# Optimization experiments

Hardware: AMD Instinct MI355X
Metric: run time of the kernel (lower is better)

Reference implementation:

```python
import jax, jax.numpy as jnp
import numpy as np

N_NODES = 50000
N_EDGES = 600000
IN_DIM = 128
FEAT = 128
N_CLS = 40


def _lin_params(key, fan_in, fan_out, bias=True):
    k1, k2 = jax.random.split(key)
    lim = 1.0 / np.sqrt(fan_in)
    W = jax.random.uniform(k1, (fan_out, fan_in), jnp.float32, -lim, lim)
    b = jax.random.uniform(k2, (fan_out,), jnp.float32, -lim, lim) if bias else None
    return W, b


def setup_inputs() -> dict:
    key = jax.random.key(0)
    ks = jax.random.split(key, 8)
    x = jax.random.normal(ks[0], (N_NODES, IN_DIM), jnp.float32)
    edge_index = jax.random.randint(ks[1], (2, N_EDGES), 0, N_NODES, jnp.int64 if jax.config.read('jax_enable_x64') else jnp.int32)
    Wl1, bl1 = _lin_params(ks[2], IN_DIM, FEAT)
    Wr1, _ = _lin_params(ks[3], IN_DIM, FEAT, bias=False)
    Wl2, bl2 = _lin_params(ks[4], FEAT, FEAT)
    Wr2, _ = _lin_params(ks[5], FEAT, FEAT, bias=False)
    Wl3, bl3 = _lin_params(ks[6], FEAT, FEAT)
    Wr3, _ = _lin_params(ks[7], FEAT, FEAT, bias=False)
    kc = jax.random.fold_in(key, 99)
    Wc, bc = _lin_params(kc, FEAT, N_CLS)
    return {"x": x, "edge_index": edge_index,
            "Wl1": Wl1, "bl1": bl1, "Wr1": Wr1,
            "Wl2": Wl2, "bl2": bl2, "Wr2": Wr2,
            "Wl3": Wl3, "bl3": bl3, "Wr3": Wr3,
            "Wc": Wc, "bc": bc}


def _sage_relu(x, src, dst, deg_inv, Wl, bl, Wr):
    # mean aggregation over incoming neighbors: gather at src, scatter-add at dst
    agg = jax.ops.segment_sum(x[src], dst, num_segments=N_NODES)  # [N, F]
    agg = agg * deg_inv[:, None]
    out = agg @ Wl.T + bl + x @ Wr.T  # W1*mean(neigh) + W2*x_root
    return jax.nn.relu(out)


def reference(x, edge_index, Wl1, bl1, Wr1, Wl2, bl2, Wr2, Wl3, bl3, Wr3, Wc, bc):
    src, dst = edge_index[0], edge_index[1]
    deg = jax.ops.segment_sum(jnp.ones((src.shape[0],), x.dtype), dst, num_segments=N_NODES)
    deg_inv = 1.0 / jnp.maximum(deg, 1.0)
    local_repr = _sage_relu(x, src, dst, deg_inv, Wl1, bl1, Wr1)
    global_repr = _sage_relu(local_repr, src, dst, deg_inv, Wl2, bl2, Wr2)
    # invariant_feature_extractor: one SAGEConvwithRelu + (eval-mode) dropout + residual
    h = _sage_relu(global_repr, src, dst, deg_inv, Wl3, bl3, Wr3)
    vanilla_if = h + global_repr
    vanilla_pred = vanilla_if @ Wc.T + bc
    return vanilla_pred
```

## Files before the change

kernel.cpp:

```cpp
#include <hip/hip_runtime.h>
#include <hip/hip_bf16.h>

constexpr int N_NODES = 50000;
constexpr int N_EDGES = 600000;
constexpr int D       = 128;
constexpr int N_CLS   = 40;

constexpr float QS = 2048.0f;
constexpr float DQ = 1.0f / 2048.0f;

using bf16x8 = __attribute__((ext_vector_type(8))) short;
using f32x4  = __attribute__((ext_vector_type(4))) float;

__device__ inline unsigned short f2bf(float f) {
    __hip_bfloat16 h = __float2bfloat16(f);
    return __builtin_bit_cast(unsigned short, h);
}
__device__ inline float bf2f(unsigned short u) {
    __hip_bfloat16 h = __builtin_bit_cast(__hip_bfloat16, u);
    return __bfloat162float(h);
}
__device__ inline short q16(float v) {
    float s = v * QS;
    s = fminf(fmaxf(s, -32767.f), 32767.f);
    return (short)__float2int_rn(s);
}


__global__ void hist_kernel(const int* __restrict__ ei, int* __restrict__ cnt) {
    int e = blockIdx.x * 256 + threadIdx.x;
    if (e < N_EDGES) atomicAdd(&cnt[ei[N_EDGES + e]], 1);
}

__global__ __launch_bounds__(1024) void scan_block_kernel(const int* __restrict__ cnt,
                                                          int* __restrict__ rs,
                                                          int* __restrict__ bsum, int n) {
    __shared__ int t[1024];
    int tid = threadIdx.x;
    int gid = blockIdx.x * 1024 + tid;
    int v = (gid < n) ? cnt[gid] : 0;
    t[tid] = v;
    __syncthreads();
    for (int off = 1; off < 1024; off <<= 1) {
        int u = (tid >= off) ? t[tid - off] : 0;
        __syncthreads();
        t[tid] += u;
        __syncthreads();
    }
    if (gid < n) rs[gid] = t[tid] - v;
    if (tid == 1023) bsum[blockIdx.x] = t[1023];
}

__global__ void finalize2_kernel(const int* __restrict__ cnt, int* __restrict__ rs,
                                 int* __restrict__ cursor, float* __restrict__ dinv,
                                 const int* __restrict__ bsum) {
    __shared__ int chunk_off;
    int tid = threadIdx.x;
    int i = blockIdx.x * 256 + tid;
    int chunk = blockIdx.x >> 2;
    if (tid < 64) {
        int v = (tid < chunk) ? bsum[tid] : 0;
#pragma unroll
        for (int o = 1; o < 64; o <<= 1) v += __shfl_xor(v, o);
        if (tid == 0) chunk_off = v;
    }
    __syncthreads();
    if (i < N_NODES) {
        int v = rs[i] + chunk_off;
        rs[i] = v;
        cursor[i] = v;
        dinv[i] = 1.0f / fmaxf((float)cnt[i], 1.0f);
        if (i == 0) rs[N_NODES] = N_EDGES;
    }
}

__global__ void scatter_kernel(const int* __restrict__ ei, int* __restrict__ cursor,
                               int* __restrict__ csr) {
    int e = blockIdx.x * 256 + threadIdx.x;
    if (e < N_EDGES) {
        int d = ei[N_EDGES + e];
        int p = atomicAdd(&cursor[d], 1);
        csr[p] = ei[e];
    }
}

__global__ void split_w3_kernel(const float* __restrict__ Wl1, const float* __restrict__ Wr1,
                                const float* __restrict__ Wl2, const float* __restrict__ Wr2,
                                const float* __restrict__ Wl3, const float* __restrict__ Wr3,
                                unsigned short* __restrict__ hi, unsigned short* __restrict__ lo) {
    int layer = blockIdx.x >> 7;
    int idx = (blockIdx.x & 127) * 256 + threadIdx.x;
    int n = idx >> 8, k = idx & 255;
    const float* Wl = (layer == 0) ? Wl1 : (layer == 1) ? Wl2 : Wl3;
    const float* Wr = (layer == 0) ? Wr1 : (layer == 1) ? Wr2 : Wr3;
    float v = (k < 128) ? Wl[n * 128 + k] : Wr[n * 128 + (k - 128)];
    unsigned short h = f2bf(v);
    size_t o = (size_t)layer * 32768 + idx;
    hi[o] = h;
    lo[o] = f2bf(v - bf2f(h));
}

__global__ void split_wc_kernel(const float* __restrict__ Wc,
                                unsigned short* __restrict__ hi, unsigned short* __restrict__ lo) {
    int idx = blockIdx.x * 256 + threadIdx.x;
    int n = idx >> 7, k = idx & 127;
    float v = (n < N_CLS) ? Wc[n * 128 + k] : 0.f;
    unsigned short h = f2bf(v);
    hi[idx] = h;
    lo[idx] = f2bf(v - bf2f(h));
}

__global__ __launch_bounds__(256) void agg_kernel(const float* __restrict__ feat,
                                                  const int* __restrict__ rs,
                                                  const int* __restrict__ csr,
                                                  const float* __restrict__ dinv,
                                                  float* __restrict__ aggn) {
    int wave = threadIdx.x >> 6;
    int lane = threadIdx.x & 63;
    int node = blockIdx.x * 4 + wave;
    if (node >= N_NODES) return;
    int e0 = rs[node], e1 = rs[node + 1];
    int half = lane >> 5;
    int fl = lane & 31;
    float ax = 0.f, ay = 0.f, az = 0.f, aw = 0.f;

    for (int base = e0; base < e1; base += 64) {
        int cnt = min(64, e1 - base);
        int idxv = (lane < cnt) ? csr[base + lane] : 0;
        int cnt2 = cnt & ~1;
        int j = 0;
        for (; j + 8 <= cnt2; j += 8) {
            int s0 = __shfl(idxv, j + half);
            int s1 = __shfl(idxv, j + 2 + half);
            int s2 = __shfl(idxv, j + 4 + half);
            int s3 = __shfl(idxv, j + 6 + half);
            float4 v0 = *(const float4*)&feat[(size_t)s0 * D + fl * 4];
            float4 v1 = *(const float4*)&feat[(size_t)s1 * D + fl * 4];
            float4 v2 = *(const float4*)&feat[(size_t)s2 * D + fl * 4];
            float4 v3 = *(const float4*)&feat[(size_t)s3 * D + fl * 4];
            ax += v0.x + v1.x + v2.x + v3.x;
            ay += v0.y + v1.y + v2.y + v3.y;
            az += v0.z + v1.z + v2.z + v3.z;
            aw += v0.w + v1.w + v2.w + v3.w;
        }
        for (; j < cnt2; j += 2) {
            int s = __shfl(idxv, j + half);
            float4 v = *(const float4*)&feat[(size_t)s * D + fl * 4];
            ax += v.x; ay += v.y; az += v.z; aw += v.w;
        }
        if (j < cnt) {
            int s = __shfl(idxv, j);
            if (half == 0) {
                float4 v = *(const float4*)&feat[(size_t)s * D + fl * 4];
                ax += v.x; ay += v.y; az += v.z; aw += v.w;
            }
        }
    }
    ax += __shfl(ax, lane ^ 32);
    ay += __shfl(ay, lane ^ 32);
    az += __shfl(az, lane ^ 32);
    aw += __shfl(aw, lane ^ 32);
    if (half == 0) {
        float di = dinv[node];
        float4 o; o.x = ax * di; o.y = ay * di; o.z = az * di; o.w = aw * di;
        *(float4*)&aggn[(size_t)node * D + fl * 4] = o;
    }
}

__global__ __launch_bounds__(256) void agg_q_kernel(const short* __restrict__ feat16,
                                                    const int* __restrict__ rs,
                                                    const int* __restrict__ csr,
                                                    const float* __restrict__ dinv,
                                                    float* __restrict__ aggn) {
    int wave = threadIdx.x >> 6;
    int lane = threadIdx.x & 63;
    int node = blockIdx.x * 4 + wave;
    if (node >= N_NODES) return;
    int e0 = rs[node], e1 = rs[node + 1];
    int q = lane >> 4;
    int fl = lane & 15;
    int acc[8] = {0, 0, 0, 0, 0, 0, 0, 0};

    auto acc8 = [&](uint4 u) {
        acc[0] += (int)(short)(u.x & 0xffff);
        acc[1] += (int)(short)(u.x >> 16);
        acc[2] += (int)(short)(u.y & 0xffff);
        acc[3] += (int)(short)(u.y >> 16);
        acc[4] += (int)(short)(u.z & 0xffff);
        acc[5] += (int)(short)(u.z >> 16);
        acc[6] += (int)(short)(u.w & 0xffff);
        acc[7] += (int)(short)(u.w >> 16);
    };

    for (int base = e0; base < e1; base += 64) {
        int cnt = min(64, e1 - base);
        int idxv = (lane < cnt) ? csr[base + lane] : 0;
        int bulk = cnt & ~15;
        int j = 0;
        for (; j < bulk; j += 16) {
            int s0 = __shfl(idxv, j + q);
            int s1 = __shfl(idxv, j + 4 + q);
            int s2 = __shfl(idxv, j + 8 + q);
            int s3 = __shfl(idxv, j + 12 + q);
            uint4 a = *(const uint4*)&feat16[(size_t)s0 * D + fl * 8];
            uint4 b = *(const uint4*)&feat16[(size_t)s1 * D + fl * 8];
            uint4 c = *(const uint4*)&feat16[(size_t)s2 * D + fl * 8];
            uint4 d = *(const uint4*)&feat16[(size_t)s3 * D + fl * 8];
            acc8(a); acc8(b); acc8(c); acc8(d);
        }
        for (; j < cnt; j += 4) {
            if (j + q < cnt) {
                int s = __shfl(idxv, j + q);
                uint4 a = *(const uint4*)&feat16[(size_t)s * D + fl * 8];
                acc8(a);
            }
        }
    }
#pragma unroll
    for (int i = 0; i < 8; ++i) {
        acc[i] += __shfl(acc[i], lane ^ 16);
        acc[i] += __shfl(acc[i], lane ^ 32);
    }
    if (q == 0) {
        float sc = dinv[node] * DQ;
        float4 o0, o1;
        o0.x = acc[0] * sc; o0.y = acc[1] * sc; o0.z = acc[2] * sc; o0.w = acc[3] * sc;
        o1.x = acc[4] * sc; o1.y = acc[5] * sc; o1.z = acc[6] * sc; o1.w = acc[7] * sc;
        *(float4*)&aggn[(size_t)node * D + fl * 8] = o0;
        *(float4*)&aggn[(size_t)node * D + fl * 8 + 4] = o1;
    }
}

__global__ __launch_bounds__(256) void gemm_mfma_kernel(const float* __restrict__ Aagg,
                                                        const float* __restrict__ Ax,
                                                        const unsigned short* __restrict__ Whi,
                                                        const unsigned short* __restrict__ Wlo,
                                                        const float* __restrict__ bias,
                                                        short* __restrict__ out16,
                                                        float* __restrict__ outp, int M) {
    __shared__ __align__(16) unsigned short AhS[64 * 32];
    __shared__ __align__(16) unsigned short AlS[64 * 32];
    __shared__ __align__(16) unsigned short WhS[128 * 32];
    __shared__ __align__(16) unsigned short WlS[128 * 32];
    char* AhB = (char*)AhS;
    char* AlB = (char*)AlS;
    char* WhB = (char*)WhS;
    char* WlB = (char*)WlS;

    int tid = threadIdx.x;
    int lane = tid & 63;
    int wid = tid >> 6;
    int wr = wid >> 1;
    int wc = wid & 1;
    int lr = lane & 15;
    int kg = (lane >> 4) * 8;
    int row0 = blockIdx.x * 64;

    f32x4 acc[2][4];
#pragma unroll
    for (int f = 0; f < 2; ++f)
#pragma unroll
        for (int j = 0; j < 4; ++j) acc[f][j] = (f32x4){0.f, 0.f, 0.f, 0.f};

    for (int kt = 0; kt < 8; ++kt) {
        const float* Asrc = (kt < 4) ? Aagg : Ax;
        int kcol = (kt & 3) * 32;

        {
            int row = tid >> 2;
            int k8 = (tid & 3) * 8;
            int gr = row0 + row;
            if (gr >= M) gr = M - 1;
            const float* p = &Asrc[(size_t)gr * D + kcol + k8];
            float4 v0 = *(const float4*)p;
            float4 v1 = *(const float4*)(p + 4);
            float fv[8] = {v0.x, v0.y, v0.z, v0.w, v1.x, v1.y, v1.z, v1.w};
            union { unsigned short u[8]; uint4 q; } ph, pl;
#pragma unroll
            for (int j = 0; j < 8; ++j) {
                unsigned short h = f2bf(fv[j]);
                ph.u[j] = h;
                pl.u[j] = f2bf(fv[j] - bf2f(h));
            }
            int boff = (row << 6) + (k8 << 1);
            boff ^= (row & 7) << 4;
            *(uint4*)(AhB + boff) = ph.q;
            *(uint4*)(AlB + boff) = pl.q;
        }
#pragma unroll
        for (int it = 0; it < 2; ++it) {
            int slot = tid + it * 256;
            int n = slot >> 2;
            int k8 = (slot & 3) * 8;
            size_t gsrc = (size_t)n * 256 + kt * 32 + k8;
            uint4 h = *(const uint4*)&Whi[gsrc];
            uint4 l = *(const uint4*)&Wlo[gsrc];
            int boff = (n << 6) + (k8 << 1);
            boff ^= (n & 7) << 4;
            *(uint4*)(WhB + boff) = h;
            *(uint4*)(WlB + boff) = l;
        }
        __syncthreads();

        {
            bf16x8 ah[2], al[2];
#pragma unroll
            for (int f = 0; f < 2; ++f) {
                int row = wr * 32 + f * 16 + lr;
                int boff = (row << 6) + (kg << 1);
                boff ^= (row & 7) << 4;
                ah[f] = *(const bf16x8*)(AhB + boff);
                al[f] = *(const bf16x8*)(AlB + boff);
            }
            bf16x8 bh[4], bl[4];
#pragma unroll
            for (int j = 0; j < 4; ++j) {
                int n = wc * 64 + j * 16 + lr;
                int boff = (n << 6) + (kg << 1);
                boff ^= (n & 7) << 4;
                bh[j] = *(const bf16x8*)(WhB + boff);
                bl[j] = *(const bf16x8*)(WlB + boff);
            }
#pragma unroll
            for (int f = 0; f < 2; ++f)
#pragma unroll
                for (int j = 0; j < 4; ++j) {
                    acc[f][j] = __builtin_amdgcn_mfma_f32_16x16x32_bf16(ah[f], bh[j], acc[f][j], 0, 0, 0);
                    acc[f][j] = __builtin_amdgcn_mfma_f32_16x16x32_bf16(ah[f], bl[j], acc[f][j], 0, 0, 0);
                    acc[f][j] = __builtin_amdgcn_mfma_f32_16x16x32_bf16(al[f], bh[j], acc[f][j], 0, 0, 0);
                }
        }
        __syncthreads();
    }

#pragma unroll
    for (int f = 0; f < 2; ++f)
#pragma unroll
        for (int j = 0; j < 4; ++j) {
            int c = wc * 64 + j * 16 + lr;
            float b = bias[c];
#pragma unroll
            for (int r = 0; r < 4; ++r) {
                int gr = row0 + wr * 32 + f * 16 + (lane >> 4) * 4 + r;
                if (gr < M) {
                    float v = fmaxf(acc[f][j][r] + b, 0.f);
                    outp[(size_t)gr * D + c] = v;
                    if (out16) out16[(size_t)gr * D + c] = q16(v);
                }
            }
        }
}

__global__ __launch_bounds__(256) void gemm_cls_kernel(const float* __restrict__ Aagg,
                                                       const float* __restrict__ Ax,
                                                       const unsigned short* __restrict__ Whi,
                                                       const unsigned short* __restrict__ Wlo,
                                                       const float* __restrict__ bias,
                                                       const float* __restrict__ residf,
                                                       const unsigned short* __restrict__ Wch,
                                                       const unsigned short* __restrict__ Wcl,
                                                       const float* __restrict__ bc,
                                                       float* __restrict__ outp, int M) {
    __shared__ __align__(16) char smem[49152];
    char* AhB = smem;
    char* AlB = smem + 8192;
    char* WhB = smem + 16384;
    char* WlB = smem + 32768;

    int tid = threadIdx.x;
    int lane = tid & 63;
    int wid = tid >> 6;
    int wr = wid >> 1;
    int wc = wid & 1;
    int lr = lane & 15;
    int kg = (lane >> 4) * 8;
    int row0 = blockIdx.x * 64;

    f32x4 acc[2][4];
#pragma unroll
    for (int f = 0; f < 2; ++f)
#pragma unroll
        for (int j = 0; j < 4; ++j) acc[f][j] = (f32x4){0.f, 0.f, 0.f, 0.f};

    for (int kt = 0; kt < 4; ++kt) {
        const float* Asrc = (kt < 2) ? Aagg : Ax;
        int kcol = (kt & 1) * 64;
#pragma unroll
        for (int it = 0; it < 2; ++it) {
            int slot = tid + it * 256;
            int row = slot >> 3;
            int k8 = (slot & 7) * 8;
            int gr = row0 + row;
            if (gr >= M) gr = M - 1;
            const float* p = &Asrc[(size_t)gr * D + kcol + k8];
            float4 v0 = *(const float4*)p;
            float4 v1 = *(const float4*)(p + 4);
            float fv[8] = {v0.x, v0.y, v0.z, v0.w, v1.x, v1.y, v1.z, v1.w};
            union { unsigned short u[8]; uint4 q; } ph, pl;
#pragma unroll
            for (int j = 0; j < 8; ++j) {
                unsigned short h = f2bf(fv[j]);
                ph.u[j] = h;
                pl.u[j] = f2bf(fv[j] - bf2f(h));
            }
            int boff = (row << 7) + (k8 << 1);
            boff ^= (row & 7) << 4;
            *(uint4*)(AhB + boff) = ph.q;
            *(uint4*)(AlB + boff) = pl.q;
        }
#pragma unroll
        for (int it = 0; it < 4; ++it) {
            int slot = tid + it * 256;
            int n = slot >> 3;
            int k8 = (slot & 7) * 8;
            size_t gsrc = (size_t)n * 256 + kt * 64 + k8;
            uint4 h = *(const uint4*)&Whi[gsrc];
            uint4 l = *(const uint4*)&Wlo[gsrc];
            int boff = (n << 7) + (k8 << 1);
            boff ^= (n & 7) << 4;
            *(uint4*)(WhB + boff) = h;
            *(uint4*)(WlB + boff) = l;
        }
        __syncthreads();
#pragma unroll
        for (int ks = 0; ks < 2; ++ks) {
            int kk = ks * 32 + kg;
            bf16x8 ah[2], al[2];
#pragma unroll
            for (int f = 0; f < 2; ++f) {
                int row = wr * 32 + f * 16 + lr;
                int boff = (row << 7) + (kk << 1);
                boff ^= (row & 7) << 4;
                ah[f] = *(const bf16x8*)(AhB + boff);
                al[f] = *(const bf16x8*)(AlB + boff);
            }
            bf16x8 bh[4], bl[4];
#pragma unroll
            for (int j = 0; j < 4; ++j) {
                int n = wc * 64 + j * 16 + lr;
                int boff = (n << 7) + (kk << 1);
                boff ^= (n & 7) << 4;
                bh[j] = *(const bf16x8*)(WhB + boff);
                bl[j] = *(const bf16x8*)(WlB + boff);
            }
#pragma unroll
            for (int f = 0; f < 2; ++f)
#pragma unroll
                for (int j = 0; j < 4; ++j) {
                    acc[f][j] = __builtin_amdgcn_mfma_f32_16x16x32_bf16(ah[f], bh[j], acc[f][j], 0, 0, 0);
                    acc[f][j] = __builtin_amdgcn_mfma_f32_16x16x32_bf16(ah[f], bl[j], acc[f][j], 0, 0, 0);
                    acc[f][j] = __builtin_amdgcn_mfma_f32_16x16x32_bf16(al[f], bh[j], acc[f][j], 0, 0, 0);
                }
        }
        __syncthreads();
    }

    f32x4 acc2[3];
#pragma unroll
    for (int j = 0; j < 3; ++j) acc2[j] = (f32x4){0.f, 0.f, 0.f, 0.f};

    for (int p = 0; p < 2; ++p) {
#pragma unroll
        for (int it = 0; it < 2; ++it) {
            int slot = tid + it * 256;
            if (slot < 384) {
                int n = slot >> 3;
                int k8 = (slot & 7) * 8;
                size_t gsrc = (size_t)n * 128 + p * 64 + k8;
                uint4 h = *(const uint4*)&Wch[gsrc];
                uint4 l = *(const uint4*)&Wcl[gsrc];
                int boff = (n << 7) + (k8 << 1);
                boff ^= (n & 7) << 4;
                *(uint4*)(WhB + boff) = h;
                *(uint4*)(WlB + boff) = l;
            }
        }
        if (wc == p) {
#pragma unroll
            for (int f = 0; f < 2; ++f)
#pragma unroll
                for (int j = 0; j < 4; ++j) {
                    int c = wc * 64 + j * 16 + lr;
                    float b = bias[c];
#pragma unroll
                    for (int r = 0; r < 4; ++r) {
                        int row = wr * 32 + f * 16 + (lane >> 4) * 4 + r;
                        int gr = row0 + row;
                        int gra = (gr < M) ? gr : (M - 1);
                        float v = fmaxf(acc[f][j][r] + b, 0.f);
                        v += residf[(size_t)gra * D + c];
                        int kloc = j * 16 + lr;
                        int boff = (row << 7) + (kloc << 1);
                        boff ^= (row & 7) << 4;
                        unsigned short h = f2bf(v);
                        *(unsigned short*)(AhB + boff) = h;
                        *(unsigned short*)(AlB + boff) = f2bf(v - bf2f(h));
                    }
                }
        }
        __syncthreads();

#pragma unroll
        for (int ks = 0; ks < 2; ++ks) {
            int kk = ks * 32 + kg;
            int row = wid * 16 + lr;
            int boffA = (row << 7) + (kk << 1);
            boffA ^= (row & 7) << 4;
            bf16x8 ah = *(const bf16x8*)(AhB + boffA);
            bf16x8 al = *(const bf16x8*)(AlB + boffA);
#pragma unroll
            for (int j = 0; j < 3; ++j) {
                int n = j * 16 + lr;
                int boffB = (n << 7) + (kk << 1);
                boffB ^= (n & 7) << 4;
                bf16x8 bh = *(const bf16x8*)(WhB + boffB);
                bf16x8 bl = *(const bf16x8*)(WlB + boffB);
                acc2[j] = __builtin_amdgcn_mfma_f32_16x16x32_bf16(ah, bh, acc2[j], 0, 0, 0);
                acc2[j] = __builtin_amdgcn_mfma_f32_16x16x32_bf16(ah, bl, acc2[j], 0, 0, 0);
                acc2[j] = __builtin_amdgcn_mfma_f32_16x16x32_bf16(al, bh, acc2[j], 0, 0, 0);
            }
        }
        __syncthreads();
    }

#pragma unroll
    for (int j = 0; j < 3; ++j) {
        int c = j * 16 + lr;
        if (c < N_CLS) {
            float b = bc[c];
#pragma unroll
            for (int r = 0; r < 4; ++r) {
                int gr = row0 + wid * 16 + (lane >> 4) * 4 + r;
                if (gr < M) outp[(size_t)gr * N_CLS + c] = acc2[j][r] + b;
            }
        }
    }
}

extern "C" void kernel_launch(void* const* d_in, const int* in_sizes, int n_in,
                              void* d_out, int out_size, void* d_ws, size_t ws_size,
                              hipStream_t stream) {
    const float* x   = (const float*)d_in[0];
    const int*   ei  = (const int*)d_in[1];
    const float* Wl1 = (const float*)d_in[2];
    const float* bl1 = (const float*)d_in[3];
    const float* Wr1 = (const float*)d_in[4];
    const float* Wl2 = (const float*)d_in[5];
    const float* bl2 = (const float*)d_in[6];
    const float* Wr2 = (const float*)d_in[7];
    const float* Wl3 = (const float*)d_in[8];
    const float* bl3 = (const float*)d_in[9];
    const float* Wr3 = (const float*)d_in[10];
    const float* Wc  = (const float*)d_in[11];
    const float* bc  = (const float*)d_in[12];
    float* out = (float*)d_out;

    char* w = (char*)d_ws;
    size_t off = 0;
    auto carve = [&](size_t bytes) -> void* {
        void* p = w + off;
        off = (off + bytes + 255) & ~(size_t)255;
        return p;
    };
    int*   cnt    = (int*)carve((size_t)N_NODES * 4);
    int*   rs     = (int*)carve((size_t)(N_NODES + 1) * 4);
    int*   cursor = (int*)carve((size_t)N_NODES * 4);
    float* dinv   = (float*)carve((size_t)N_NODES * 4);
    int*   bsum   = (int*)carve(64 * 4);
    int*   csr    = (int*)carve((size_t)N_EDGES * 4);
    float* aggn   = (float*)carve((size_t)N_NODES * D * 4);
    float* bufA   = (float*)carve((size_t)N_NODES * D * 4);
    float* bufB   = (float*)carve((size_t)N_NODES * D * 4);
    short* t16    = (short*)carve((size_t)N_NODES * D * 2);
    unsigned short* w123h = (unsigned short*)carve(3 * 128 * 256 * 2);
    unsigned short* w123l = (unsigned short*)carve(3 * 128 * 256 * 2);
    unsigned short* wch   = (unsigned short*)carve(48 * 128 * 2);
    unsigned short* wcl   = (unsigned short*)carve(48 * 128 * 2);
    (void)ws_size;

    const int NBLK_SCAN = (N_NODES + 1023) / 1024;
    const int GRID_E = (N_EDGES + 255) / 256;
    const int GRID_N = (N_NODES + 255) / 256;
    const int GRID_AGG = (N_NODES + 3) / 4;
    const int GRID_GEMM = (N_NODES + 63) / 64;

    hipMemsetAsync(cnt, 0, (size_t)N_NODES * 4, stream);
    hipLaunchKernelGGL(hist_kernel, dim3(GRID_E), dim3(256), 0, stream, ei, cnt);
    hipLaunchKernelGGL(split_w3_kernel, dim3(384), dim3(256), 0, stream,
                       Wl1, Wr1, Wl2, Wr2, Wl3, Wr3, w123h, w123l);
    hipLaunchKernelGGL(split_wc_kernel, dim3(24), dim3(256), 0, stream, Wc, wch, wcl);
    hipLaunchKernelGGL(scan_block_kernel, dim3(NBLK_SCAN), dim3(1024), 0, stream, cnt, rs, bsum, N_NODES);
    hipLaunchKernelGGL(finalize2_kernel, dim3(GRID_N), dim3(256), 0, stream, cnt, rs, cursor, dinv, bsum);
    hipLaunchKernelGGL(scatter_kernel, dim3(GRID_E), dim3(256), 0, stream, ei, cursor, csr);

    hipLaunchKernelGGL(agg_kernel, dim3(GRID_AGG), dim3(256), 0, stream, x, rs, csr, dinv, aggn);
    hipLaunchKernelGGL(gemm_mfma_kernel, dim3(GRID_GEMM), dim3(256), 0, stream,
                       aggn, x, w123h, w123l, bl1, (short*)nullptr, bufA, N_NODES);
    hipLaunchKernelGGL(agg_kernel, dim3(GRID_AGG), dim3(256), 0, stream, bufA, rs, csr, dinv, aggn);
    hipLaunchKernelGGL(gemm_mfma_kernel, dim3(GRID_GEMM), dim3(256), 0, stream,
                       aggn, bufA, w123h + 32768, w123l + 32768, bl2, t16, bufB, N_NODES);
    hipLaunchKernelGGL(agg_q_kernel, dim3(GRID_AGG), dim3(256), 0, stream, t16, rs, csr, dinv, aggn);
    hipLaunchKernelGGL(gemm_cls_kernel, dim3(GRID_GEMM), dim3(256), 0, stream,
                       aggn, bufB, w123h + 65536, w123l + 65536, bl3, bufB,
                       wch, wcl, bc, out, N_NODES);
}
```

Measured before the change: 341.4 us.

## Prefetch GEMM operands into registers and double-buffer A tile in LDS

The layer GEMM kernel stops staging weights through shared memory. Each wave now loads its bf16 hi/lo weight fragments straight from global memory into registers. A and weight loads for the next k-tile are issued before the MFMAs of the current tile, A is double-buffered in LDS, and the two barriers per iteration become one. The aim is to hide global load latency and cut LDS traffic and synchronisation, at the cost of more registers and redundant weight reads across waves, which rely on L1/L2.

```diff
diff --git a/kernel.cpp b/kernel.cpp
--- a/kernel.cpp
+++ b/kernel.cpp
@@ -231,21 +231,15 @@
     }
 }
 
-__global__ __launch_bounds__(256) void gemm_mfma_kernel(const float* __restrict__ Aagg,
-                                                        const float* __restrict__ Ax,
-                                                        const unsigned short* __restrict__ Whi,
-                                                        const unsigned short* __restrict__ Wlo,
-                                                        const float* __restrict__ bias,
-                                                        short* __restrict__ out16,
-                                                        float* __restrict__ outp, int M) {
-    __shared__ __align__(16) unsigned short AhS[64 * 32];
-    __shared__ __align__(16) unsigned short AlS[64 * 32];
-    __shared__ __align__(16) unsigned short WhS[128 * 32];
-    __shared__ __align__(16) unsigned short WlS[128 * 32];
-    char* AhB = (char*)AhS;
-    char* AlB = (char*)AlS;
-    char* WhB = (char*)WhS;
-    char* WlB = (char*)WlS;
+__global__ __launch_bounds__(256) void gemm_v2_kernel(const float* __restrict__ Aagg,
+                                                      const float* __restrict__ Ax,
+                                                      const unsigned short* __restrict__ Whi,
+                                                      const unsigned short* __restrict__ Wlo,
+                                                      const float* __restrict__ bias,
+                                                      short* __restrict__ out16,
+                                                      float* __restrict__ outp, int M) {
+    __shared__ __align__(16) unsigned short AhS[2][64 * 32];
+    __shared__ __align__(16) unsigned short AlS[2][64 * 32];
 
     int tid = threadIdx.x;
     int lane = tid & 63;
@@ -256,25 +250,46 @@
     int kg = (lane >> 4) * 8;
     int row0 = blockIdx.x * 64;
 
+    int arow = tid >> 2;
+    int ak8 = (tid & 3) * 8;
+    int agr = row0 + arow;
+    if (agr >= M) agr = M - 1;
+    const float* aag = &Aagg[(size_t)agr * D + ak8];
+    const float* axp = &Ax[(size_t)agr * D + ak8];
+    int aboff = (arow << 6) + (ak8 << 1);
+    aboff ^= (arow & 7) << 4;
+
+    const unsigned short* whp[4];
+    const unsigned short* wlp[4];
+#pragma unroll
+    for (int j = 0; j < 4; ++j) {
+        int n = wc * 64 + j * 16 + lr;
+        whp[j] = &Whi[n * 256 + kg];
+        wlp[j] = &Wlo[n * 256 + kg];
+    }
+
     f32x4 acc[2][4];
 #pragma unroll
     for (int f = 0; f < 2; ++f)
 #pragma unroll
         for (int j = 0; j < 4; ++j) acc[f][j] = (f32x4){0.f, 0.f, 0.f, 0.f};
 
+    float4 a0c = *(const float4*)(aag);
+    float4 a1c = *(const float4*)(aag + 4);
+    bf16x8 whc[4], wlc[4];
+#pragma unroll
+    for (int j = 0; j < 4; ++j) {
+        whc[j] = *(const bf16x8*)(whp[j]);
+        wlc[j] = *(const bf16x8*)(wlp[j]);
+    }
+
+#pragma unroll
     for (int kt = 0; kt < 8; ++kt) {
-        const float* Asrc = (kt < 4) ? Aagg : Ax;
-        int kcol = (kt & 3) * 32;
+        unsigned short* AhB = AhS[kt & 1];
+        unsigned short* AlB = AlS[kt & 1];
 
         {
-            int row = tid >> 2;
-            int k8 = (tid & 3) * 8;
-            int gr = row0 + row;
-            if (gr >= M) gr = M - 1;
-            const float* p = &Asrc[(size_t)gr * D + kcol + k8];
-            float4 v0 = *(const float4*)p;
-            float4 v1 = *(const float4*)(p + 4);
-            float fv[8] = {v0.x, v0.y, v0.z, v0.w, v1.x, v1.y, v1.z, v1.w};
+            float fv[8] = {a0c.x, a0c.y, a0c.z, a0c.w, a1c.x, a1c.y, a1c.z, a1c.w};
             union { unsigned short u[8]; uint4 q; } ph, pl;
 #pragma unroll
             for (int j = 0; j < 8; ++j) {
@@ -282,25 +297,29 @@
                 ph.u[j] = h;
                 pl.u[j] = f2bf(fv[j] - bf2f(h));
             }
-            int boff = (row << 6) + (k8 << 1);
-            boff ^= (row & 7) << 4;
-            *(uint4*)(AhB + boff) = ph.q;
-            *(uint4*)(AlB + boff) = pl.q;
-        }
-#pragma unroll
-        for (int it = 0; it < 2; ++it) {
-            int slot = tid + it * 256;
-            int n = slot >> 2;
-            int k8 = (slot & 3) * 8;
-            size_t gsrc = (size_t)n * 256 + kt * 32 + k8;
-            uint4 h = *(const uint4*)&Whi[gsrc];
-            uint4 l = *(const uint4*)&Wlo[gsrc];
-            int boff = (n << 6) + (k8 << 1);
-            boff ^= (n & 7) << 4;
-            *(uint4*)(WhB + boff) = h;
-            *(uint4*)(WlB + boff) = l;
-        }
-        __syncthreads();
+            *(uint4*)((char*)AhB + aboff) = ph.q;
+            *(uint4*)((char*)AlB + aboff) = pl.q;
+        }
+
+        float4 a0n, a1n;
+        bf16x8 whn[4], wln[4];
+        if (kt < 7) {
+            int ktn = kt + 1;
+            const float* src = (ktn < 4) ? aag : axp;
+            int kcol = (ktn & 3) * 32;
+            a0n = *(const float4*)(src + kcol);
+            a1n = *(const float4*)(src + kcol + 4);
+            int wof = ktn * 32;
+#pragma unroll
+            for (int j = 0; j < 4; ++j) {
+                whn[j] = *(const bf16x8*)(whp[j] + wof);
+                wln[j] = *(const bf16x8*)(wlp[j] + wof);
+            }
+        }
+
+        asm volatile("s_waitcnt lgkmcnt(0)" ::: "memory");
+        __builtin_amdgcn_s_barrier();
+        asm volatile("" ::: "memory");
 
         {
             bf16x8 ah[2], al[2];
@@ -309,28 +328,24 @@
                 int row = wr * 32 + f * 16 + lr;
                 int boff = (row << 6) + (kg << 1);
                 boff ^= (row & 7) << 4;
-                ah[f] = *(const bf16x8*)(AhB + boff);
-                al[f] = *(const bf16x8*)(AlB + boff);
-            }
-            bf16x8 bh[4], bl[4];
-#pragma unroll
-            for (int j = 0; j < 4; ++j) {
-                int n = wc * 64 + j * 16 + lr;
-                int boff = (n << 6) + (kg << 1);
-                boff ^= (n & 7) << 4;
-                bh[j] = *(const bf16x8*)(WhB + boff);
-                bl[j] = *(const bf16x8*)(WlB + boff);
+                ah[f] = *(const bf16x8*)((char*)AhB + boff);
+                al[f] = *(const bf16x8*)((char*)AlB + boff);
             }
 #pragma unroll
             for (int f = 0; f < 2; ++f)
 #pragma unroll
                 for (int j = 0; j < 4; ++j) {
-                    acc[f][j] = __builtin_amdgcn_mfma_f32_16x16x32_bf16(ah[f], bh[j], acc[f][j], 0, 0, 0);
-                    acc[f][j] = __builtin_amdgcn_mfma_f32_16x16x32_bf16(ah[f], bl[j], acc[f][j], 0, 0, 0);
-                    acc[f][j] = __builtin_amdgcn_mfma_f32_16x16x32_bf16(al[f], bh[j], acc[f][j], 0, 0, 0);
+                    acc[f][j] = __builtin_amdgcn_mfma_f32_16x16x32_bf16(ah[f], whc[j], acc[f][j], 0, 0, 0);
+                    acc[f][j] = __builtin_amdgcn_mfma_f32_16x16x32_bf16(ah[f], wlc[j], acc[f][j], 0, 0, 0);
+                    acc[f][j] = __builtin_amdgcn_mfma_f32_16x16x32_bf16(al[f], whc[j], acc[f][j], 0, 0, 0);
                 }
         }
-        __syncthreads();
+
+        if (kt < 7) {
+            a0c = a0n; a1c = a1n;
+#pragma unroll
+            for (int j = 0; j < 4; ++j) { whc[j] = whn[j]; wlc[j] = wln[j]; }
+        }
     }
 
 #pragma unroll
@@ -594,10 +609,10 @@
     hipLaunchKernelGGL(scatter_kernel, dim3(GRID_E), dim3(256), 0, stream, ei, cursor, csr);
 
     hipLaunchKernelGGL(agg_kernel, dim3(GRID_AGG), dim3(256), 0, stream, x, rs, csr, dinv, aggn);
-    hipLaunchKernelGGL(gemm_mfma_kernel, dim3(GRID_GEMM), dim3(256), 0, stream,
+    hipLaunchKernelGGL(gemm_v2_kernel, dim3(GRID_GEMM), dim3(256), 0, stream,
                        aggn, x, w123h, w123l, bl1, (short*)nullptr, bufA, N_NODES);
     hipLaunchKernelGGL(agg_kernel, dim3(GRID_AGG), dim3(256), 0, stream, bufA, rs, csr, dinv, aggn);
-    hipLaunchKernelGGL(gemm_mfma_kernel, dim3(GRID_GEMM), dim3(256), 0, stream,
+    hipLaunchKernelGGL(gemm_v2_kernel, dim3(GRID_GEMM), dim3(256), 0, stream,
                        aggn, bufA, w123h + 32768, w123l + 32768, bl2, t16, bufB, N_NODES);
     hipLaunchKernelGGL(agg_q_kernel, dim3(GRID_AGG), dim3(256), 0, stream, t16, rs, csr, dinv, aggn);
     hipLaunchKernelGGL(gemm_cls_kernel, dim3(GRID_GEMM), dim3(256), 0, stream,
```

After: 374.2 us. 9.6% more time.
